# Kernel optimization log

Measured on AMD Instinct MI355X. Metric: run time of the kernel, lower is better.

Reference implementation:

```python
import jax, jax.numpy as jnp
import numpy as np

N, F_IN, F_OUT = 8192, 512, 256


def setup_inputs() -> dict:
    key = jax.random.key(0)
    k1, k2, k3, k4 = jax.random.split(key, 4)
    x = jax.random.normal(k1, (N, F_IN), dtype=jnp.float32)
    adj = jax.random.randint(k2, (N, N), 0, 2, dtype=jnp.int32)
    # xavier_uniform with gain=1.414
    limW = 1.414 * np.sqrt(6.0 / (F_IN + F_OUT))
    W = jax.random.uniform(k3, (F_IN, F_OUT), dtype=jnp.float32, minval=-limW, maxval=limW)
    lima = 1.414 * np.sqrt(6.0 / (2 * F_OUT + 1))
    a = jax.random.uniform(k4, (2 * F_OUT, 1), dtype=jnp.float32, minval=-lima, maxval=lima)
    return {"x": x, "adj": adj, "W": W, "a": a}


def reference(x, adj, W, a):
    # h = x @ W : [N, F_out]
    h = x @ W
    f_out = h.shape[1]
    # additive score a^T [h_i ; h_j] is separable: (h @ a_l)_i + (h @ a_r)_j
    f_src = h @ a[:f_out, 0]   # [N]
    f_dst = h @ a[f_out:, 0]   # [N]
    e = jax.nn.leaky_relu(f_src[:, None] + f_dst[None, :], negative_slope=0.2)  # [N, N]
    e = jnp.where(adj > 0, e, jnp.float32(-9e15))
    attention = jax.nn.softmax(e, axis=1)  # row-wise over neighbors
    # dropout(p=0.6) is identity in eval mode
    h_prime = attention @ h  # [N, F_out]
    return h_prime
```

## Files before the change

### kernel.cpp

```cpp
#include <hip/hip_runtime.h>
#include <hip/hip_bf16.h>

#define NN 8192
#define FIN 512
#define FOUT 256

typedef __attribute__((ext_vector_type(8))) short short8;
typedef __attribute__((ext_vector_type(4))) float float4v;
typedef __attribute__((ext_vector_type(16))) float float16v;

__device__ __forceinline__ short f2bf(float f) {
    union { float f; unsigned u; } v; v.f = f;
    unsigned r = (v.u + 0x7FFFu + ((v.u >> 16) & 1u)) >> 16;
    return (short)r;
}

__global__ __launch_bounds__(256) void pack_kernel(const int* __restrict__ adj,
                                                   unsigned long long* __restrict__ pk64) {
    const int tid = blockIdx.x * 256 + threadIdx.x;
    const int stride = 2048 * 256;
#pragma unroll 8
    for (int k = 0; k < (NN * NN) / stride; ++k) {
        int idx = tid + k * stride;
        unsigned long long m = __ballot(adj[idx] != 0);
        if ((threadIdx.x & 63) == 0) pk64[idx >> 6] = m;
    }
}

__global__ __launch_bounds__(256) void wt_kernel(const float* __restrict__ W,
                                                 short* __restrict__ Wt) {
    __shared__ short tile[32][33];
    int tx = threadIdx.x & 31, ty = threadIdx.x >> 5;
    int k0 = blockIdx.x * 32, n0 = blockIdx.y * 32;
#pragma unroll
    for (int r = 0; r < 32; r += 8)
        tile[ty + r][tx] = f2bf(W[(size_t)(k0 + ty + r) * FOUT + n0 + tx]);
    __syncthreads();
#pragma unroll
    for (int r = 0; r < 32; r += 8)
        Wt[(size_t)(n0 + ty + r) * FIN + k0 + tx] = tile[tx][ty + r];
}

__global__ __launch_bounds__(256) void h_kernel(const float* __restrict__ x,
                                                const short* __restrict__ Wt,
                                                const float* __restrict__ a,
                                                short* __restrict__ h_t,
                                                float* __restrict__ f_src,
                                                float* __restrict__ f_dst) {
    int wave = (blockIdx.x << 2) + (threadIdx.x >> 6);
    int lane = threadIdx.x & 63;
    int m0 = (wave & 511) << 4;
    int n0 = (wave >> 9) << 6;
    int lr = lane & 15, lq = lane >> 4;

    const float* xrow = x + (size_t)(m0 + lr) * FIN + lq * 8;
    const short* wbase = Wt + (size_t)(n0 + lr) * FIN + lq * 8;

    float4v acc[4] = {};
    for (int k0 = 0; k0 < FIN; k0 += 32) {
        float4v xa = *(const float4v*)(xrow + k0);
        float4v xb = *(const float4v*)(xrow + k0 + 4);
        short8 av;
        av[0] = f2bf(xa[0]); av[1] = f2bf(xa[1]); av[2] = f2bf(xa[2]); av[3] = f2bf(xa[3]);
        av[4] = f2bf(xb[0]); av[5] = f2bf(xb[1]); av[6] = f2bf(xb[2]); av[7] = f2bf(xb[3]);
#pragma unroll
        for (int ct = 0; ct < 4; ct++) {
            short8 bv = *(const short8*)(wbase + (size_t)ct * 16 * FIN + k0);
            acc[ct] = __builtin_amdgcn_mfma_f32_16x16x32_bf16(av, bv, acc[ct], 0, 0, 0);
        }
    }
    float s_part[4] = {0.f, 0.f, 0.f, 0.f};
    float d_part[4] = {0.f, 0.f, 0.f, 0.f};
#pragma unroll
    for (int ct = 0; ct < 4; ct++) {
        int n = n0 + ct * 16 + lr;
        float al = a[n], ar = a[FOUT + n];
#pragma unroll
        for (int reg = 0; reg < 4; reg++) {
            float hv = acc[ct][reg];
            s_part[reg] = fmaf(hv, al, s_part[reg]);
            d_part[reg] = fmaf(hv, ar, d_part[reg]);
            h_t[(size_t)n * NN + (m0 + lq * 4 + reg)] = f2bf(hv);
        }
    }
#pragma unroll
    for (int off = 1; off < 16; off <<= 1) {
#pragma unroll
        for (int reg = 0; reg < 4; reg++) {
            s_part[reg] += __shfl_xor(s_part[reg], off);
            d_part[reg] += __shfl_xor(d_part[reg], off);
        }
    }
    const float LOG2E = 1.4426950408889634f;
    if (lr == 0) {
#pragma unroll
        for (int reg = 0; reg < 4; reg++) {
            atomicAdd(&f_src[m0 + lq * 4 + reg], s_part[reg] * LOG2E);
            atomicAdd(&f_dst[m0 + lq * 4 + reg], d_part[reg] * LOG2E);
        }
    }
}

__global__ __launch_bounds__(512, 4) void gat_kernel(const unsigned long long* __restrict__ pk64,
                                                     const short* __restrict__ h_t,
                                                     const float* __restrict__ f_src,
                                                     const float* __restrict__ f_dst,
                                                     float* __restrict__ Opart,
                                                     float* __restrict__ lpart,
                                                     int jlen) {
    __shared__ short Ht[2][256 * 64];

    const int t = threadIdx.x;
    const int lane = t & 63;
    const int w = t >> 6;
    const int l31 = lane & 31, lq = lane >> 5;
    const int wr = w & 3, wc = w >> 2;
    const int i0 = blockIdx.x * 128;
    const int slice = blockIdx.y;
    const int jbase = slice * jlen;
    const int r = i0 + wr * 32 + l31;
    const int nchunk = jlen >> 6;
    const int rsw = l31 & 7;

    const float fs = f_src[r];
    const unsigned long long* pkRow = pk64 + (size_t)r * (NN / 64) + (jbase >> 6);
    const float* fdL = f_dst + jbase + lq * 8;

    const int sf = t >> 1, sq0 = (t & 1) * 4;
    const short* hrow = h_t + (size_t)sf * NN + jbase + sq0 * 8;
    const int fsw = sf & 7;
    short* HtW = &Ht[0][sf * 64];

    float16v acc[4] = {};
    float lp = 0.f;

    {
        short8 s0 = *(const short8*)(hrow + 0);
        short8 s1 = *(const short8*)(hrow + 8);
        short8 s2 = *(const short8*)(hrow + 16);
        short8 s3 = *(const short8*)(hrow + 24);
        *(short8*)(HtW + (((sq0 + 0) ^ fsw) << 3)) = s0;
        *(short8*)(HtW + (((sq0 + 1) ^ fsw) << 3)) = s1;
        *(short8*)(HtW + (((sq0 + 2) ^ fsw) << 3)) = s2;
        *(short8*)(HtW + (((sq0 + 3) ^ fsw) << 3)) = s3;
    }
    unsigned long long bm = pkRow[0];
    __syncthreads();

    for (int c = 0; c < nchunk; ++c) {
        const int cn = (c + 1 < nchunk) ? c + 1 : 0;
        short8 s0 = *(const short8*)(hrow + cn * 64 + 0);
        short8 s1 = *(const short8*)(hrow + cn * 64 + 8);
        short8 s2 = *(const short8*)(hrow + cn * 64 + 16);
        short8 s3 = *(const short8*)(hrow + cn * 64 + 24);
        unsigned long long bmn = pkRow[cn];

        const short* HtR = &Ht[c & 1][0];
        const unsigned bmlo = (unsigned)bm, bmhi = (unsigned)(bm >> 32);
#pragma unroll
        for (int kk = 0; kk < 4; ++kk) {
            const int jo = c * 64 + kk * 16;
            float4 f0 = *(const float4*)(fdL + jo);
            float4 f1 = *(const float4*)(fdL + jo + 4);
            unsigned w32 = (kk < 2) ? bmlo : bmhi;
            unsigned m8 = (w32 >> ((kk & 1) * 16 + lq * 8)) & 0xffu;

            short8 af;
            const float* ff0 = (const float*)&f0;
            const float* ff1 = (const float*)&f1;
#pragma unroll
            for (int q = 0; q < 8; ++q) {
                float fdv = (q < 4) ? ff0[q] : ff1[q - 4];
                float y = fs + fdv;
                y = fmaxf(y, 0.2f * y);
                float e = exp2f(y);
                float p = (m8 & (1u << q)) ? e : 0.f;
                lp += p;
                af[q] = f2bf(p);
            }
            const int cb = ((kk * 2 + lq) ^ rsw) << 3;
#pragma unroll
            for (int nt = 0; nt < 4; nt++) {
                const int feat = wc * 128 + nt * 32 + l31;
                short8 b = *(const short8*)(HtR + feat * 64 + cb);
                acc[nt] = __builtin_amdgcn_mfma_f32_32x32x16_bf16(af, b, acc[nt], 0, 0, 0);
            }
        }
        short* HtN = &Ht[(c & 1) ^ 1][sf * 64];
        *(short8*)(HtN + (((sq0 + 0) ^ fsw) << 3)) = s0;
        *(short8*)(HtN + (((sq0 + 1) ^ fsw) << 3)) = s1;
        *(short8*)(HtN + (((sq0 + 2) ^ fsw) << 3)) = s2;
        *(short8*)(HtN + (((sq0 + 3) ^ fsw) << 3)) = s3;
        bm = bmn;
        __syncthreads();
    }

    lp += __shfl_xor(lp, 32);
    if (wc == 0 && lq == 0) lpart[(size_t)slice * NN + r] = lp;

    float* ob = Opart + ((size_t)slice * NN + i0 + wr * 32) * FOUT + wc * 128;
#pragma unroll
    for (int nt = 0; nt < 4; nt++) {
        int n = nt * 32 + l31;
#pragma unroll
        for (int reg = 0; reg < 16; reg++) {
            int row = (reg & 3) + 8 * (reg >> 2) + 4 * lq;
            ob[(size_t)row * FOUT + n] = acc[nt][reg];
        }
    }
}

__global__ __launch_bounds__(256) void combine_kernel(const float* __restrict__ Opart,
                                                      const float* __restrict__ lpart,
                                                      float* __restrict__ out, int slices) {
    int i = blockIdx.x, n = threadIdx.x;
    float o = 0.f, l = 0.f;
    for (int s = 0; s < slices; s++) {
        o += Opart[((size_t)s * NN + i) * FOUT + n];
        l += lpart[(size_t)s * NN + i];
    }
    out[(size_t)i * FOUT + n] = o / l;
}

extern "C" void kernel_launch(void* const* d_in, const int* in_sizes, int n_in,
                              void* d_out, int out_size, void* d_ws, size_t ws_size,
                              hipStream_t stream) {
    const float* x   = (const float*)d_in[0];
    const int*   adj = (const int*)d_in[1];
    const float* W   = (const float*)d_in[2];
    const float* a   = (const float*)d_in[3];
    float* out = (float*)d_out;

    char* ws = (char*)d_ws;
    short* h_t   = (short*)ws;
    short* Wt    = (short*)(ws + (4u << 20));
    float* f_src = (float*)(ws + (4u << 20) + (256u << 10));
    float* f_dst = (float*)(ws + (4u << 20) + (288u << 10));
    float* lpart = (float*)(ws + (4u << 20) + (320u << 10));
    unsigned long long* pk64 = (unsigned long long*)(ws + (6u << 20));
    float* Opart = (float*)(ws + (16u << 20));

    const int slices = 8;
    const int jlen = NN / slices;

    hipMemsetAsync(f_src, 0, 2 * NN * sizeof(float), stream);
    pack_kernel<<<2048, 256, 0, stream>>>(adj, pk64);
    wt_kernel<<<dim3(FIN / 32, FOUT / 32), 256, 0, stream>>>(W, Wt);
    h_kernel<<<512, 256, 0, stream>>>(x, Wt, a, h_t, f_src, f_dst);
    gat_kernel<<<dim3(NN / 128, slices), 512, 0, stream>>>(pk64, h_t, f_src, f_dst,
                                                           Opart, lpart, jlen);
    combine_kernel<<<NN, 256, 0, stream>>>(Opart, lpart, out, slices);
}
```

Measured before the change: 524.3 us.

## Fuse adjacency bit-packing into attention kernel and single-buffer the h tile

Removes the separate pack kernel and its 8 MB bitmask round trip. Each attention block now ballots its own 128x1024 slice of the int32 adjacency into a shared-memory mask table before the main loop. The h tile drops from a double buffer to a single buffer with an extra barrier per chunk, which frees LDS for the mask table but serialises the LDS fill with the MFMA work. The adjacency read is unchanged in total, but it now sits at the head of every block instead of in a streaming pre-pass.

Result: slower. 571.7 us (+9.0%).

```diff
diff --git a/kernel.cpp b/kernel.cpp
--- a/kernel.cpp
+++ b/kernel.cpp
@@ -4,6 +4,9 @@
 #define NN 8192
 #define FIN 512
 #define FOUT 256
+#define SLICES 8
+#define JLEN (NN / SLICES)
+#define NCHUNK (JLEN / 64)
 
 typedef __attribute__((ext_vector_type(8))) short short8;
 typedef __attribute__((ext_vector_type(4))) float float4v;
@@ -13,18 +16,6 @@
     union { float f; unsigned u; } v; v.f = f;
     unsigned r = (v.u + 0x7FFFu + ((v.u >> 16) & 1u)) >> 16;
     return (short)r;
-}
-
-__global__ __launch_bounds__(256) void pack_kernel(const int* __restrict__ adj,
-                                                   unsigned long long* __restrict__ pk64) {
-    const int tid = blockIdx.x * 256 + threadIdx.x;
-    const int stride = 2048 * 256;
-#pragma unroll 8
-    for (int k = 0; k < (NN * NN) / stride; ++k) {
-        int idx = tid + k * stride;
-        unsigned long long m = __ballot(adj[idx] != 0);
-        if ((threadIdx.x & 63) == 0) pk64[idx >> 6] = m;
-    }
 }
 
 __global__ __launch_bounds__(256) void wt_kernel(const float* __restrict__ W,
@@ -101,14 +92,14 @@
     }
 }
 
-__global__ __launch_bounds__(512, 4) void gat_kernel(const unsigned long long* __restrict__ pk64,
+__global__ __launch_bounds__(512, 4) void gat_kernel(const int* __restrict__ adj,
                                                      const short* __restrict__ h_t,
                                                      const float* __restrict__ f_src,
                                                      const float* __restrict__ f_dst,
                                                      float* __restrict__ Opart,
-                                                     float* __restrict__ lpart,
-                                                     int jlen) {
-    __shared__ short Ht[2][256 * 64];
+                                                     float* __restrict__ lpart) {
+    __shared__ short Ht[256 * 64];
+    __shared__ unsigned long long msk[128 * 17];
 
     const int t = threadIdx.x;
     const int lane = t & 63;
@@ -117,45 +108,52 @@
     const int wr = w & 3, wc = w >> 2;
     const int i0 = blockIdx.x * 128;
     const int slice = blockIdx.y;
-    const int jbase = slice * jlen;
+    const int jbase = slice * JLEN;
     const int r = i0 + wr * 32 + l31;
-    const int nchunk = jlen >> 6;
     const int rsw = l31 & 7;
 
+    {
+        const int* ab = adj + (size_t)(i0 + (w << 4)) * NN + jbase + lane;
+#pragma unroll 8
+        for (int u = 0; u < 256; ++u) {
+            int row = u >> 4, c = u & 15;
+            int v = ab[(size_t)row * NN + c * 64];
+            unsigned long long m = __ballot(v != 0);
+            if (lane == 0) msk[((w << 4) + row) * 17 + c] = m;
+        }
+    }
+
     const float fs = f_src[r];
-    const unsigned long long* pkRow = pk64 + (size_t)r * (NN / 64) + (jbase >> 6);
     const float* fdL = f_dst + jbase + lq * 8;
 
     const int sf = t >> 1, sq0 = (t & 1) * 4;
     const short* hrow = h_t + (size_t)sf * NN + jbase + sq0 * 8;
     const int fsw = sf & 7;
-    short* HtW = &Ht[0][sf * 64];
+    short* HtW = &Ht[sf * 64];
 
     float16v acc[4] = {};
     float lp = 0.f;
 
-    {
-        short8 s0 = *(const short8*)(hrow + 0);
-        short8 s1 = *(const short8*)(hrow + 8);
-        short8 s2 = *(const short8*)(hrow + 16);
-        short8 s3 = *(const short8*)(hrow + 24);
+    short8 s0 = *(const short8*)(hrow + 0);
+    short8 s1 = *(const short8*)(hrow + 8);
+    short8 s2 = *(const short8*)(hrow + 16);
+    short8 s3 = *(const short8*)(hrow + 24);
+    __syncthreads();
+
+    for (int c = 0; c < NCHUNK; ++c) {
         *(short8*)(HtW + (((sq0 + 0) ^ fsw) << 3)) = s0;
         *(short8*)(HtW + (((sq0 + 1) ^ fsw) << 3)) = s1;
         *(short8*)(HtW + (((sq0 + 2) ^ fsw) << 3)) = s2;
         *(short8*)(HtW + (((sq0 + 3) ^ fsw) << 3)) = s3;
-    }
-    unsigned long long bm = pkRow[0];
-    __syncthreads();
-
-    for (int c = 0; c < nchunk; ++c) {
-        const int cn = (c + 1 < nchunk) ? c + 1 : 0;
-        short8 s0 = *(const short8*)(hrow + cn * 64 + 0);
-        short8 s1 = *(const short8*)(hrow + cn * 64 + 8);
-        short8 s2 = *(const short8*)(hrow + cn * 64 + 16);
-        short8 s3 = *(const short8*)(hrow + cn * 64 + 24);
-        unsigned long long bmn = pkRow[cn];
-
-        const short* HtR = &Ht[c & 1][0];
+        __syncthreads();
+
+        const int cn = (c + 1 < NCHUNK) ? c + 1 : c;
+        s0 = *(const short8*)(hrow + cn * 64 + 0);
+        s1 = *(const short8*)(hrow + cn * 64 + 8);
+        s2 = *(const short8*)(hrow + cn * 64 + 16);
+        s3 = *(const short8*)(hrow + cn * 64 + 24);
+
+        const unsigned long long bm = msk[(wr * 32 + l31) * 17 + c];
         const unsigned bmlo = (unsigned)bm, bmhi = (unsigned)(bm >> 32);
 #pragma unroll
         for (int kk = 0; kk < 4; ++kk) {
@@ -182,16 +180,10 @@
 #pragma unroll
             for (int nt = 0; nt < 4; nt++) {
                 const int feat = wc * 128 + nt * 32 + l31;
-                short8 b = *(const short8*)(HtR + feat * 64 + cb);
+                short8 b = *(const short8*)(&Ht[0] + feat * 64 + cb);
                 acc[nt] = __builtin_amdgcn_mfma_f32_32x32x16_bf16(af, b, acc[nt], 0, 0, 0);
             }
         }
-        short* HtN = &Ht[(c & 1) ^ 1][sf * 64];
-        *(short8*)(HtN + (((sq0 + 0) ^ fsw) << 3)) = s0;
-        *(short8*)(HtN + (((sq0 + 1) ^ fsw) << 3)) = s1;
-        *(short8*)(HtN + (((sq0 + 2) ^ fsw) << 3)) = s2;
-        *(short8*)(HtN + (((sq0 + 3) ^ fsw) << 3)) = s3;
-        bm = bmn;
         __syncthreads();
     }
 
@@ -212,10 +204,11 @@
 
 __global__ __launch_bounds__(256) void combine_kernel(const float* __restrict__ Opart,
                                                       const float* __restrict__ lpart,
-                                                      float* __restrict__ out, int slices) {
+                                                      float* __restrict__ out) {
     int i = blockIdx.x, n = threadIdx.x;
     float o = 0.f, l = 0.f;
-    for (int s = 0; s < slices; s++) {
+#pragma unroll
+    for (int s = 0; s < SLICES; s++) {
         o += Opart[((size_t)s * NN + i) * FOUT + n];
         l += lpart[(size_t)s * NN + i];
     }
@@ -237,17 +230,12 @@
     float* f_src = (float*)(ws + (4u << 20) + (256u << 10));
     float* f_dst = (float*)(ws + (4u << 20) + (288u << 10));
     float* lpart = (float*)(ws + (4u << 20) + (320u << 10));
-    unsigned long long* pk64 = (unsigned long long*)(ws + (6u << 20));
     float* Opart = (float*)(ws + (16u << 20));
 
-    const int slices = 8;
-    const int jlen = NN / slices;
-
     hipMemsetAsync(f_src, 0, 2 * NN * sizeof(float), stream);
-    pack_kernel<<<2048, 256, 0, stream>>>(adj, pk64);
     wt_kernel<<<dim3(FIN / 32, FOUT / 32), 256, 0, stream>>>(W, Wt);
     h_kernel<<<512, 256, 0, stream>>>(x, Wt, a, h_t, f_src, f_dst);
-    gat_kernel<<<dim3(NN / 128, slices), 512, 0, stream>>>(pk64, h_t, f_src, f_dst,
-                                                           Opart, lpart, jlen);
-    combine_kernel<<<NN, 256, 0, stream>>>(Opart, lpart, out, slices);
-}
+    gat_kernel<<<dim3(NN / 128, SLICES), 512, 0, stream>>>(adj, h_t, f_src, f_dst,
+                                                           Opart, lpart);
+    combine_kernel<<<NN, 256, 0, stream>>>(Opart, lpart, out);
+}
```
